# Kernel optimization log

Hardware: AMD Instinct MI355X
Metric: run time of the kernel (lower is better)

Reference implementation:

```python
import jax, jax.numpy as jnp
import numpy as np

B_, CIN, HH, WW = 2, 64, 64, 64
D_MODEL, D_INNER, D_STATE, DT_RANK, D_CONV = 64, 128, 16, 32, 3


def setup_inputs() -> dict:
    key = jax.random.key(0)
    ks = jax.random.split(key, 16)
    w = lambda k, shape: jax.random.normal(k, shape, jnp.float32) * 0.05
    # dt_proj bias init (torch: inv-softplus of dt sampled in [dt_min, dt_max])
    dt = jnp.exp(jax.random.uniform(ks[10], (D_INNER,)) * (np.log(0.1) - np.log(0.001)) + np.log(0.001))
    dt = jnp.clip(dt, 1e-4, None)
    inv_dt = dt + jnp.log(-jnp.expm1(-dt))
    A = jnp.tile(jnp.arange(1, D_STATE + 1, dtype=jnp.float32), (D_INNER, 1))
    return {
        "rgb_feat": jax.random.normal(ks[0], (B_, CIN, HH, WW), jnp.float32),
        "dte_feat": jax.random.normal(ks[1], (B_, CIN, HH, WW), jnp.float32),
        "conv1_w": w(ks[2], (D_MODEL, CIN)), "conv1_b": jnp.zeros((D_MODEL,), jnp.float32),
        "conv2_w": w(ks[3], (D_MODEL, CIN)), "conv2_b": jnp.zeros((D_MODEL,), jnp.float32),
        "conv3_w": w(ks[4], (CIN, D_MODEL)), "conv3_b": jnp.zeros((CIN,), jnp.float32),
        "norm_w": jnp.ones((D_MODEL,), jnp.float32),
        "in_proj_w": w(ks[5], (2 * D_INNER, D_MODEL)),
        "conv1d_w": w(ks[6], (D_INNER, D_CONV)), "conv1d_b": jnp.zeros((D_INNER,), jnp.float32),
        "x_proj_w": w(ks[7], (DT_RANK + 2 * D_STATE, D_INNER)),
        "dt_proj_w": jax.random.uniform(ks[8], (D_INNER, DT_RANK), jnp.float32, -DT_RANK ** -0.5, DT_RANK ** -0.5),
        "dt_proj_b": inv_dt,
        "A_log": jnp.log(A),
        "Dp": jnp.ones((D_INNER,), jnp.float32),
        "out_proj_w": w(ks[9], (D_MODEL, D_INNER)),
    }


def _conv1x1(x, w, b):
    return jnp.einsum('bchw,oc->bohw', x, w) + b[None, :, None, None]


def _rmsnorm(x, w, eps=1e-5):
    return x * jax.lax.rsqrt(jnp.mean(x * x, axis=-1, keepdims=True) + eps) * w


def _dwconv1d(x, w, b):
    # x: [B,L,D]; depthwise conv, kernel 3, padding 1 (same length)
    xt = jnp.transpose(x, (0, 2, 1))  # [B,D,L]
    y = jax.lax.conv_general_dilated(xt, w[:, None, :], (1,), [(1, 1)],
                                     dimension_numbers=('NCH', 'OIH', 'NCH'),
                                     feature_group_count=D_INNER)
    return jnp.transpose(y + b[None, :, None], (0, 2, 1))


def _mamba(x, h, p):
    # x: [B,L,d_model]
    xz = x @ p['in_proj_w'].T                      # [B,L,2*d_inner]
    xc, z = jnp.split(xz, 2, axis=-1)
    xc = jax.nn.silu(_dwconv1d(xc, p['conv1d_w'], p['conv1d_b']))
    A = -jnp.exp(p['A_log'])                       # [D,S]
    dbc = xc @ p['x_proj_w'].T                     # [B,L,dt_rank+2S]
    delta, Bm, Cm = jnp.split(dbc, [DT_RANK, DT_RANK + D_STATE], axis=-1)
    delta = jax.nn.softplus(delta @ p['dt_proj_w'].T + p['dt_proj_b'])  # [B,L,D]
    deltaA = jnp.exp(delta[..., None] * A)         # [B,L,D,S]
    BX = delta[..., None] * Bm[:, :, None, :] * xc[..., None]  # [B,L,D,S]
    h = deltaA * h + BX
    y = jnp.einsum('blds,bls->bld', h, Cm) + p['Dp'] * xc
    out = (y * jax.nn.silu(z)) @ p['out_proj_w'].T
    return out, h


def _residual_block(x4d, h, p):
    B, C, H, W = x4d.shape
    x = jnp.transpose(x4d.reshape(B, C, H * W), (0, 2, 1))  # [B,L,C]
    x = _rmsnorm(x, p['norm_w'])
    out, h = _mamba(x, h, p)
    out = out + x
    return jnp.transpose(out, (0, 2, 1)).reshape(B, C, H, W), h


def _rsfm(rgb_feat, dte_feat, conv1_w, conv1_b, conv2_w, conv2_b, conv3_w, conv3_b,
          norm_w, in_proj_w, conv1d_w, conv1d_b, x_proj_w, dt_proj_w, dt_proj_b,
          A_log, Dp, out_proj_w):
    p = dict(norm_w=norm_w, in_proj_w=in_proj_w, conv1d_w=conv1d_w, conv1d_b=conv1d_b,
             x_proj_w=x_proj_w, dt_proj_w=dt_proj_w, dt_proj_b=dt_proj_b,
             A_log=A_log, Dp=Dp, out_proj_w=out_proj_w)
    rgb = _conv1x1(rgb_feat, conv1_w, conv1_b)
    dte = _conv1x1(dte_feat, conv2_w, conv2_b)
    B = rgb.shape[0]
    h = jnp.zeros((B, HH * WW, D_INNER, D_STATE), jnp.float32)
    out1, h = _residual_block(rgb, h, p)
    out2, h = _residual_block(dte + out1, h, p)
    out3, h = _residual_block(rgb + out2, h, p)
    out4, h = _residual_block(dte + out3, h, p)
    out5, h = _residual_block(rgb + out4, h, p)
    out6, h = _residual_block(dte + out5, h, p)
    return _conv1x1(out6, conv3_w, conv3_b), h


def reference(rgb_feat, dte_feat, conv1_w, conv1_b, conv2_w, conv2_b, conv3_w, conv3_b,
              norm_w, in_proj_w, conv1d_w, conv1d_b, x_proj_w, dt_proj_w, dt_proj_b,
              A_log, Dp, out_proj_w):
    return _rsfm(rgb_feat, dte_feat, conv1_w, conv1_b, conv2_w, conv2_b, conv3_w, conv3_b,
                 norm_w, in_proj_w, conv1d_w, conv1d_b, x_proj_w, dt_proj_w, dt_proj_b,
                 A_log, Dp, out_proj_w)
```

## Files before the change

kernel.cpp:

```cpp
#include <hip/hip_runtime.h>

#define LSEQ 4096
#define NPOS 8192

__device__ __forceinline__ float silu_f(float x){ return x / (1.f + __expf(-x)); }
__device__ __forceinline__ float softplus_f(float x){
  return fmaxf(x, 0.f) + log1pf(__expf(-fabsf(x)));
}

__global__ __launch_bounds__(256) void k_prep(
    const float* __restrict__ ipw, const float* __restrict__ xpw,
    const float* __restrict__ dtw, const float* __restrict__ opw,
    const float* __restrict__ w1, const float* __restrict__ w2,
    const float* __restrict__ w3, const float* __restrict__ alog,
    float* __restrict__ ipT, float* __restrict__ xpT,
    float* __restrict__ dtT, float* __restrict__ opT,
    float* __restrict__ w1T, float* __restrict__ w2T,
    float* __restrict__ w3T, float* __restrict__ Aneg)
{
  int t = blockIdx.x * 256 + threadIdx.x;
  if (t < 16384){ int o = t >> 6, c = t & 63; ipT[c * 256 + o] = ipw[t]; }
  if (t < 8192){ int o = t >> 7, d = t & 127; xpT[d * 64 + o] = xpw[t]; }
  if (t < 4096){ int d = t >> 5, r = t & 31; dtT[r * 128 + d] = dtw[t]; }
  if (t < 8192){ int o = t >> 7, d = t & 127; opT[d * 64 + o] = opw[t]; }
  if (t < 4096){ int o = t >> 6, c = t & 63;
                 w1T[c*64+o] = w1[t]; w2T[c*64+o] = w2[t]; w3T[c*64+o] = w3[t]; }
  if (t < 2048){ Aneg[t] = -__expf(alog[t]); }
}

__global__ __launch_bounds__(256) void k_convin(
    const float* __restrict__ rgb, const float* __restrict__ dte,
    const float* __restrict__ w1T, const float* __restrict__ b1,
    const float* __restrict__ w2T, const float* __restrict__ b2,
    float* __restrict__ rgbp, float* __restrict__ dtep)
{
  int gw = (blockIdx.x * 256 + threadIdx.x) >> 6;
  int lane = threadIdx.x & 63;
  int which = gw >> 13;
  int n = gw & 8191;
  const float* x  = which ? dte : rgb;
  const float* wT = which ? w2T : w1T;
  const float* bb = which ? b2 : b1;
  float* o = which ? dtep : rgbp;
  int b = n >> 12, l = n & 4095;
  const float* xp = x + (size_t)b * 262144 + l;
  float acc = bb[lane];
  for (int c = 0; c < 64; c++)
    acc += wT[c*64 + lane] * xp[(size_t)c * 4096];
  o[(size_t)n*64 + lane] = acc;
}

__global__ __launch_bounds__(256) void k_pre(
    const float* __restrict__ xin, const float* __restrict__ normw,
    const float* __restrict__ ipT,
    float* __restrict__ xn, float* __restrict__ xcp, float* __restrict__ zs)
{
  __shared__ __align__(16) float xnl[4][8][64];
  const int wv = threadIdx.x >> 6, lane = threadIdx.x & 63;
  const int n0 = (blockIdx.x * 4 + wv) * 8;
  float nw = normw[lane];
  #pragma unroll 1
  for (int p = 0; p < 8; p++){
    int n = n0 + p;
    float v = xin[(size_t)n*64 + lane];
    float ss = v * v;
    for (int m = 32; m > 0; m >>= 1) ss += __shfl_xor(ss, m);
    v = v * rsqrtf(ss * (1.f/64.f) + 1e-5f) * nw;
    xn[(size_t)n*64 + lane] = v;
    xnl[wv][p][lane] = v;
  }
  float ac[8][4] = {};
  for (int c = 0; c < 64; c++){
    float w0 = ipT[c*256 + lane],       w1 = ipT[c*256 + 64 + lane];
    float w2 = ipT[c*256 + 128 + lane], w3 = ipT[c*256 + 192 + lane];
    #pragma unroll
    for (int p = 0; p < 8; p++){
      float xv = xnl[wv][p][c];
      ac[p][0] += w0*xv; ac[p][1] += w1*xv; ac[p][2] += w2*xv; ac[p][3] += w3*xv;
    }
  }
  #pragma unroll
  for (int p = 0; p < 8; p++){
    int n = n0 + p;
    xcp[(size_t)n*128 + lane]      = ac[p][0];
    xcp[(size_t)n*128 + 64 + lane] = ac[p][1];
    zs[(size_t)n*128 + lane]       = silu_f(ac[p][2]);
    zs[(size_t)n*128 + 64 + lane]  = silu_f(ac[p][3]);
  }
}

__global__ __launch_bounds__(256) void k_step(
    const float* __restrict__ xcpA, float* __restrict__ xcpB,
    float* __restrict__ zs, float* __restrict__ xn,
    float* __restrict__ h, const float* __restrict__ base_next,
    const float* __restrict__ xpT, const float* __restrict__ dtT,
    const float* __restrict__ opT, const float* __restrict__ Aneg,
    const float* __restrict__ c1w, const float* __restrict__ c1b,
    const float* __restrict__ dtb, const float* __restrict__ Dpw,
    const float* __restrict__ normw, const float* __restrict__ ipT,
    int hasH, int fusePre)
{
  __shared__ __align__(16) float xcl[4][4][128];
  __shared__ __align__(16) float dbl[4][4][64];
  __shared__ __align__(16) float yzl[4][4][128];
  __shared__ __align__(16) float xnl[4][4][64];
  const int wv = threadIdx.x >> 6, lane = threadIdx.x & 63;
  const int n0 = (blockIdx.x * 4 + wv) * 4;
  const int d0 = lane, d1 = 64 + lane;

  float cw00 = c1w[d0*3+0], cw01 = c1w[d0*3+1], cw02 = c1w[d0*3+2];
  float cw10 = c1w[d1*3+0], cw11 = c1w[d1*3+1], cw12 = c1w[d1*3+2];
  float cb0 = c1b[d0], cb1 = c1b[d1];

  float xc[4][2];
  #pragma unroll
  for (int p = 0; p < 4; p++){
    int n = n0 + p, l = n & (LSEQ-1);
    const float* xr = xcpA + (size_t)n * 128;
    float am0 = (l > 0) ? xr[d0 - 128] : 0.f;
    float am1 = (l > 0) ? xr[d1 - 128] : 0.f;
    float a00 = xr[d0], a01 = xr[d1];
    float ap0 = (l < LSEQ-1) ? xr[d0 + 128] : 0.f;
    float ap1 = (l < LSEQ-1) ? xr[d1 + 128] : 0.f;
    float v0 = silu_f(cw00*am0 + cw01*a00 + cw02*ap0 + cb0);
    float v1 = silu_f(cw10*am1 + cw11*a01 + cw12*ap1 + cb1);
    xc[p][0] = v0; xc[p][1] = v1;
    xcl[wv][p][d0] = v0; xcl[wv][p][d1] = v1;
  }

  float xa0=0.f, xa1=0.f, xa2=0.f, xa3=0.f;
  for (int d = 0; d < 128; d++){
    float w = xpT[d*64 + lane];
    xa0 += w * xcl[wv][0][d];
    xa1 += w * xcl[wv][1][d];
    xa2 += w * xcl[wv][2][d];
    xa3 += w * xcl[wv][3][d];
  }
  dbl[wv][0][lane]=xa0; dbl[wv][1][lane]=xa1; dbl[wv][2][lane]=xa2; dbl[wv][3][lane]=xa3;

  float tb0 = dtb[d0], tb1 = dtb[d1];
  float da[4][2];
  #pragma unroll
  for (int p = 0; p < 4; p++){ da[p][0]=tb0; da[p][1]=tb1; }
  for (int r = 0; r < 32; r++){
    float w0 = dtT[r*128 + d0];
    float w1 = dtT[r*128 + d1];
    #pragma unroll
    for (int p = 0; p < 4; p++){
      float bv = dbl[wv][p][r];
      da[p][0] += w0 * bv; da[p][1] += w1 * bv;
    }
  }
  float dl[4][2];
  #pragma unroll
  for (int p = 0; p < 4; p++){ dl[p][0]=softplus_f(da[p][0]); dl[p][1]=softplus_f(da[p][1]); }

  float an0[16], an1[16];
  {
    const float4* A0 = (const float4*)(Aneg + d0*16);
    const float4* A1 = (const float4*)(Aneg + d1*16);
    #pragma unroll
    for (int q = 0; q < 4; q++){
      float4 a = A0[q]; an0[q*4+0]=a.x; an0[q*4+1]=a.y; an0[q*4+2]=a.z; an0[q*4+3]=a.w;
      float4 b = A1[q]; an1[q*4+0]=b.x; an1[q*4+1]=b.y; an1[q*4+2]=b.z; an1[q*4+3]=b.w;
    }
  }
  float dp0 = Dpw[d0], dp1 = Dpw[d1];

  #pragma unroll 1
  for (int p = 0; p < 4; p++){
    int n = n0 + p;
    float Bm[16], Cm[16];
    {
      const float4* bb = (const float4*)&dbl[wv][p][32];
      const float4* cc = (const float4*)&dbl[wv][p][48];
      #pragma unroll
      for (int q = 0; q < 4; q++){
        float4 a = bb[q]; Bm[q*4+0]=a.x; Bm[q*4+1]=a.y; Bm[q*4+2]=a.z; Bm[q*4+3]=a.w;
        float4 b = cc[q]; Cm[q*4+0]=b.x; Cm[q*4+1]=b.y; Cm[q*4+2]=b.z; Cm[q*4+3]=b.w;
      }
    }
    float* hp0 = h + ((size_t)n*2048 + (size_t)d0*16);
    float* hp1 = h + ((size_t)n*2048 + (size_t)d1*16);
    float h0[16], h1[16];
    if (hasH){
      #pragma unroll
      for (int q = 0; q < 4; q++){
        float4 v = ((const float4*)hp0)[q];
        h0[q*4+0]=v.x; h0[q*4+1]=v.y; h0[q*4+2]=v.z; h0[q*4+3]=v.w;
        float4 w = ((const float4*)hp1)[q];
        h1[q*4+0]=w.x; h1[q*4+1]=w.y; h1[q*4+2]=w.z; h1[q*4+3]=w.w;
      }
    } else {
      #pragma unroll
      for (int s = 0; s < 16; s++){ h0[s]=0.f; h1[s]=0.f; }
    }
    float y0 = 0.f, y1 = 0.f;
    float dl0 = dl[p][0], dl1 = dl[p][1];
    float bx0 = dl0 * xc[p][0], bx1 = dl1 * xc[p][1];
    #pragma unroll
    for (int s = 0; s < 16; s++){
      h0[s] = __expf(dl0*an0[s])*h0[s] + bx0*Bm[s];
      y0 += h0[s]*Cm[s];
      h1[s] = __expf(dl1*an1[s])*h1[s] + bx1*Bm[s];
      y1 += h1[s]*Cm[s];
    }
    #pragma unroll
    for (int q = 0; q < 4; q++){
      float4 v; v.x=h0[q*4+0]; v.y=h0[q*4+1]; v.z=h0[q*4+2]; v.w=h0[q*4+3];
      ((float4*)hp0)[q] = v;
      float4 w; w.x=h1[q*4+0]; w.y=h1[q*4+1]; w.z=h1[q*4+2]; w.w=h1[q*4+3];
      ((float4*)hp1)[q] = w;
    }
    y0 += dp0 * xc[p][0];
    y1 += dp1 * xc[p][1];
    yzl[wv][p][d0] = y0 * zs[(size_t)n*128 + d0];
    yzl[wv][p][d1] = y1 * zs[(size_t)n*128 + d1];
  }

  float oa[4] = {0.f,0.f,0.f,0.f};
  for (int d = 0; d < 128; d++){
    float w = opT[d*64 + lane];
    oa[0] += w * yzl[wv][0][d];
    oa[1] += w * yzl[wv][1][d];
    oa[2] += w * yzl[wv][2][d];
    oa[3] += w * yzl[wv][3][d];
  }

  float nw = normw[lane];
  if (fusePre){
    #pragma unroll 1
    for (int p = 0; p < 4; p++){
      int n = n0 + p;
      float v = oa[p] + xn[(size_t)n*64 + lane] + base_next[(size_t)n*64 + lane];
      float ss = v * v;
      for (int m = 32; m > 0; m >>= 1) ss += __shfl_xor(ss, m);
      v = v * rsqrtf(ss * (1.f/64.f) + 1e-5f) * nw;
      xn[(size_t)n*64 + lane] = v;
      xnl[wv][p][lane] = v;
    }
    float ac[4][4] = {};
    for (int c = 0; c < 64; c++){
      float w0 = ipT[c*256 + lane],       w1 = ipT[c*256 + 64 + lane];
      float w2 = ipT[c*256 + 128 + lane], w3 = ipT[c*256 + 192 + lane];
      #pragma unroll
      for (int p = 0; p < 4; p++){
        float xv = xnl[wv][p][c];
        ac[p][0] += w0*xv; ac[p][1] += w1*xv; ac[p][2] += w2*xv; ac[p][3] += w3*xv;
      }
    }
    #pragma unroll
    for (int p = 0; p < 4; p++){
      int n = n0 + p;
      xcpB[(size_t)n*128 + lane]      = ac[p][0];
      xcpB[(size_t)n*128 + 64 + lane] = ac[p][1];
      zs[(size_t)n*128 + lane]        = silu_f(ac[p][2]);
      zs[(size_t)n*128 + 64 + lane]   = silu_f(ac[p][3]);
    }
  } else {
    #pragma unroll
    for (int p = 0; p < 4; p++){
      int n = n0 + p;
      xcpB[(size_t)n*64 + lane] = oa[p] + xn[(size_t)n*64 + lane];
    }
  }
}

__global__ __launch_bounds__(256) void k_conv3(
    const float* __restrict__ out6, const float* __restrict__ w3T,
    const float* __restrict__ b3, float* __restrict__ out)
{
  __shared__ __align__(16) float t[64][65];
  const int tid = threadIdx.x;
  const int n0 = blockIdx.x * 64;
  #pragma unroll
  for (int i = 0; i < 16; i++){
    int idx = tid + 256*i;
    int r = idx >> 6, c = idx & 63;
    t[r][c] = out6[(size_t)(n0 + r)*64 + c];
  }
  __syncthreads();
  const int i = tid & 63;
  const int cb = (tid >> 6) * 16;
  float acc[16];
  #pragma unroll
  for (int j = 0; j < 16; j++) acc[j] = b3[cb + j];
  for (int o = 0; o < 64; o++){
    float xv = t[i][o];
    #pragma unroll
    for (int j = 0; j < 16; j++) acc[j] += w3T[o*64 + cb + j] * xv;
  }
  const int b = n0 >> 12;
  const int l = (n0 & 4095) + i;
  #pragma unroll
  for (int j = 0; j < 16; j++)
    out[(size_t)b*262144 + (size_t)(cb + j)*4096 + l] = acc[j];
}

extern "C" void kernel_launch(void* const* d_in, const int* in_sizes, int n_in,
                              void* d_out, int out_size, void* d_ws, size_t ws_size,
                              hipStream_t stream)
{
  const float* rgb  = (const float*)d_in[0];
  const float* dte  = (const float*)d_in[1];
  const float* w1   = (const float*)d_in[2];
  const float* b1   = (const float*)d_in[3];
  const float* w2   = (const float*)d_in[4];
  const float* b2   = (const float*)d_in[5];
  const float* w3   = (const float*)d_in[6];
  const float* b3   = (const float*)d_in[7];
  const float* nrm  = (const float*)d_in[8];
  const float* ipw  = (const float*)d_in[9];
  const float* c1w  = (const float*)d_in[10];
  const float* c1b  = (const float*)d_in[11];
  const float* xpw  = (const float*)d_in[12];
  const float* dtw  = (const float*)d_in[13];
  const float* dtb  = (const float*)d_in[14];
  const float* alog = (const float*)d_in[15];
  const float* Dpw  = (const float*)d_in[16];
  const float* opw  = (const float*)d_in[17];

  float* out  = (float*)d_out;
  float* hbuf = out + 524288;

  float* ws   = (float*)d_ws;
  float* rgbp = ws;
  float* dtep = ws + 524288;
  float* xnb  = ws + 1048576;
  float* zsb  = ws + 1572864;
  float* xcp0 = ws + 2621440;
  float* xcp1 = ws + 3670016;
  float* Aneg = ws + 4718592;
  float* wb   = ws + 4720640;
  float* ipT = wb;
  float* xpT = wb + 16384;
  float* dtT = wb + 24576;
  float* opT = wb + 28672;
  float* w1T = wb + 36864;
  float* w2T = wb + 40960;
  float* w3T = wb + 45056;

  k_prep<<<64, 256, 0, stream>>>(ipw, xpw, dtw, opw, w1, w2, w3, alog,
                                 ipT, xpT, dtT, opT, w1T, w2T, w3T, Aneg);
  k_convin<<<4096, 256, 0, stream>>>(rgb, dte, w1T, b1, w2T, b2, rgbp, dtep);
  k_pre<<<256, 256, 0, stream>>>(rgbp, nrm, ipT, xnb, xcp0, zsb);

  float* xa[2] = {xcp0, xcp1};
  for (int k = 0; k < 6; k++){
    const float* base = (k == 5) ? nullptr : ((k & 1) ? rgbp : dtep);
    k_step<<<512, 256, 0, stream>>>(xa[k & 1], xa[(k & 1) ^ 1], zsb, xnb, hbuf, base,
                                    xpT, dtT, opT, Aneg, c1w, c1b, dtb, Dpw, nrm, ipT,
                                    (k > 0) ? 1 : 0, (k < 5) ? 1 : 0);
  }
  k_conv3<<<128, 256, 0, stream>>>(xcp0, w3T, b3, out);
}
```

Baseline: 417.4 us.

## Store intermediate SSM state in bf16, tile input conv, and halve positions per wave

The 64 MB-scale hidden state h is kept in a bf16 workspace between residual blocks, and only the final block writes fp32 to the output. This roughly halves the dominant HBM traffic of the step kernels. The input 1x1 convs are rewritten to stage a 64-position tile in LDS and write coalesced outputs. k_pre and k_step now process 2 positions per wave instead of 8/4, launching more blocks for better occupancy. Rounding h to bf16 between blocks adds precision error that may break tolerance.

Measured after the change: 364.4 us. 12.7% less time.

```diff
diff --git a/kernel.cpp b/kernel.cpp
--- a/kernel.cpp
+++ b/kernel.cpp
@@ -1,8 +1,27 @@
 #include <hip/hip_runtime.h>
+
+typedef unsigned short u16;
+typedef unsigned int u32;
 
 #define LSEQ 4096
 #define NPOS 8192
 
+__device__ __forceinline__ float bf2f(u16 u){
+  union { u32 i; float f; } v; v.i = ((u32)u) << 16; return v.f;
+}
+__device__ __forceinline__ u16 f2bf(float f){
+  union { float f; u32 i; } v; v.f = f;
+  u32 x = v.i;
+  return (u16)((x + 0x7fffu + ((x >> 16) & 1u)) >> 16);
+}
+__device__ __forceinline__ float2 up2(u32 u){
+  union { u32 i; float f; } a, b;
+  a.i = u << 16; b.i = u & 0xffff0000u;
+  float2 r; r.x = a.f; r.y = b.f; return r;
+}
+__device__ __forceinline__ u32 pk2(float a, float b){
+  return (u32)f2bf(a) | ((u32)f2bf(b) << 16);
+}
 __device__ __forceinline__ float silu_f(float x){ return x / (1.f + __expf(-x)); }
 __device__ __forceinline__ float softplus_f(float x){
   return fmaxf(x, 0.f) + log1pf(__expf(-fabsf(x)));
@@ -34,20 +53,44 @@
     const float* __restrict__ w2T, const float* __restrict__ b2,
     float* __restrict__ rgbp, float* __restrict__ dtep)
 {
-  int gw = (blockIdx.x * 256 + threadIdx.x) >> 6;
-  int lane = threadIdx.x & 63;
-  int which = gw >> 13;
-  int n = gw & 8191;
-  const float* x  = which ? dte : rgb;
-  const float* wT = which ? w2T : w1T;
-  const float* bb = which ? b2 : b1;
+  __shared__ __align__(16) float xt[64][64];
+  __shared__ __align__(16) float ot[64][65];
+  const int tid = threadIdx.x;
+  const int which = blockIdx.x & 1;
+  const int n0 = (blockIdx.x >> 1) * 64;
+  const int b = n0 >> 12, l0 = n0 & 4095;
+  const float* src = which ? dte : rgb;
+  const float* wT  = which ? w2T : w1T;
+  const float* bb  = which ? b2 : b1;
   float* o = which ? dtep : rgbp;
-  int b = n >> 12, l = n & 4095;
-  const float* xp = x + (size_t)b * 262144 + l;
-  float acc = bb[lane];
-  for (int c = 0; c < 64; c++)
-    acc += wT[c*64 + lane] * xp[(size_t)c * 4096];
-  o[(size_t)n*64 + lane] = acc;
+
+  #pragma unroll
+  for (int j = 0; j < 16; j++){
+    int idx = tid + 256 * j;
+    int c = idx >> 6, p = idx & 63;
+    xt[c][p] = src[(size_t)b * 262144 + (size_t)c * 4096 + l0 + p];
+  }
+  __syncthreads();
+
+  const int pos = tid & 63;
+  const int cb  = (tid >> 6) * 16;
+  float acc[16];
+  #pragma unroll
+  for (int j = 0; j < 16; j++) acc[j] = bb[cb + j];
+  for (int c = 0; c < 64; c++){
+    float xv = xt[c][pos];
+    #pragma unroll
+    for (int j = 0; j < 16; j++) acc[j] += wT[c*64 + cb + j] * xv;
+  }
+  #pragma unroll
+  for (int j = 0; j < 16; j++) ot[pos][cb + j] = acc[j];
+  __syncthreads();
+  #pragma unroll
+  for (int j = 0; j < 16; j++){
+    int idx = tid + 256 * j;
+    int p = idx >> 6, c = idx & 63;
+    o[(size_t)(n0 + p)*64 + c] = ot[p][c];
+  }
 }
 
 __global__ __launch_bounds__(256) void k_pre(
@@ -55,12 +98,12 @@
     const float* __restrict__ ipT,
     float* __restrict__ xn, float* __restrict__ xcp, float* __restrict__ zs)
 {
-  __shared__ __align__(16) float xnl[4][8][64];
+  __shared__ __align__(16) float xnl[4][2][64];
   const int wv = threadIdx.x >> 6, lane = threadIdx.x & 63;
-  const int n0 = (blockIdx.x * 4 + wv) * 8;
+  const int n0 = (blockIdx.x * 4 + wv) * 2;
   float nw = normw[lane];
-  #pragma unroll 1
-  for (int p = 0; p < 8; p++){
+  #pragma unroll
+  for (int p = 0; p < 2; p++){
     int n = n0 + p;
     float v = xin[(size_t)n*64 + lane];
     float ss = v * v;
@@ -69,18 +112,18 @@
     xn[(size_t)n*64 + lane] = v;
     xnl[wv][p][lane] = v;
   }
-  float ac[8][4] = {};
+  float ac[2][4] = {};
   for (int c = 0; c < 64; c++){
     float w0 = ipT[c*256 + lane],       w1 = ipT[c*256 + 64 + lane];
     float w2 = ipT[c*256 + 128 + lane], w3 = ipT[c*256 + 192 + lane];
     #pragma unroll
-    for (int p = 0; p < 8; p++){
+    for (int p = 0; p < 2; p++){
       float xv = xnl[wv][p][c];
       ac[p][0] += w0*xv; ac[p][1] += w1*xv; ac[p][2] += w2*xv; ac[p][3] += w3*xv;
     }
   }
   #pragma unroll
-  for (int p = 0; p < 8; p++){
+  for (int p = 0; p < 2; p++){
     int n = n0 + p;
     xcp[(size_t)n*128 + lane]      = ac[p][0];
     xcp[(size_t)n*128 + 64 + lane] = ac[p][1];
@@ -92,7 +135,8 @@
 __global__ __launch_bounds__(256) void k_step(
     const float* __restrict__ xcpA, float* __restrict__ xcpB,
     float* __restrict__ zs, float* __restrict__ xn,
-    float* __restrict__ h, const float* __restrict__ base_next,
+    u16* __restrict__ hbf, float* __restrict__ hfin,
+    const float* __restrict__ base_next,
     const float* __restrict__ xpT, const float* __restrict__ dtT,
     const float* __restrict__ opT, const float* __restrict__ Aneg,
     const float* __restrict__ c1w, const float* __restrict__ c1b,
@@ -100,60 +144,59 @@
     const float* __restrict__ normw, const float* __restrict__ ipT,
     int hasH, int fusePre)
 {
-  __shared__ __align__(16) float xcl[4][4][128];
-  __shared__ __align__(16) float dbl[4][4][64];
-  __shared__ __align__(16) float yzl[4][4][128];
-  __shared__ __align__(16) float xnl[4][4][64];
+  __shared__ __align__(16) float xcl[4][2][128];
+  __shared__ __align__(16) float dbl[4][2][64];
+  __shared__ __align__(16) float yzl[4][2][128];
+  __shared__ __align__(16) float xnl[4][2][64];
   const int wv = threadIdx.x >> 6, lane = threadIdx.x & 63;
-  const int n0 = (blockIdx.x * 4 + wv) * 4;
+  const int n0 = (blockIdx.x * 4 + wv) * 2;
   const int d0 = lane, d1 = 64 + lane;
 
   float cw00 = c1w[d0*3+0], cw01 = c1w[d0*3+1], cw02 = c1w[d0*3+2];
   float cw10 = c1w[d1*3+0], cw11 = c1w[d1*3+1], cw12 = c1w[d1*3+2];
   float cb0 = c1b[d0], cb1 = c1b[d1];
 
-  float xc[4][2];
-  #pragma unroll
-  for (int p = 0; p < 4; p++){
-    int n = n0 + p, l = n & (LSEQ-1);
+  float xc0[2], xc1[2];
+  #pragma unroll
+  for (int p = 0; p < 2; p++){
+    int n = n0 + p, l = n & 4095;
     const float* xr = xcpA + (size_t)n * 128;
-    float am0 = (l > 0) ? xr[d0 - 128] : 0.f;
-    float am1 = (l > 0) ? xr[d1 - 128] : 0.f;
+    float am0 = 0.f, am1 = 0.f, ap0 = 0.f, ap1 = 0.f;
+    if (l > 0)    { am0 = xr[d0 - 128]; am1 = xr[d1 - 128]; }
     float a00 = xr[d0], a01 = xr[d1];
-    float ap0 = (l < LSEQ-1) ? xr[d0 + 128] : 0.f;
-    float ap1 = (l < LSEQ-1) ? xr[d1 + 128] : 0.f;
+    if (l < 4095) { ap0 = xr[d0 + 128]; ap1 = xr[d1 + 128]; }
     float v0 = silu_f(cw00*am0 + cw01*a00 + cw02*ap0 + cb0);
     float v1 = silu_f(cw10*am1 + cw11*a01 + cw12*ap1 + cb1);
-    xc[p][0] = v0; xc[p][1] = v1;
+    xc0[p] = v0; xc1[p] = v1;
     xcl[wv][p][d0] = v0; xcl[wv][p][d1] = v1;
   }
 
-  float xa0=0.f, xa1=0.f, xa2=0.f, xa3=0.f;
-  for (int d = 0; d < 128; d++){
-    float w = xpT[d*64 + lane];
-    xa0 += w * xcl[wv][0][d];
-    xa1 += w * xcl[wv][1][d];
-    xa2 += w * xcl[wv][2][d];
-    xa3 += w * xcl[wv][3][d];
-  }
-  dbl[wv][0][lane]=xa0; dbl[wv][1][lane]=xa1; dbl[wv][2][lane]=xa2; dbl[wv][3][lane]=xa3;
-
-  float tb0 = dtb[d0], tb1 = dtb[d1];
-  float da[4][2];
-  #pragma unroll
-  for (int p = 0; p < 4; p++){ da[p][0]=tb0; da[p][1]=tb1; }
-  for (int r = 0; r < 32; r++){
-    float w0 = dtT[r*128 + d0];
-    float w1 = dtT[r*128 + d1];
-    #pragma unroll
-    for (int p = 0; p < 4; p++){
-      float bv = dbl[wv][p][r];
-      da[p][0] += w0 * bv; da[p][1] += w1 * bv;
-    }
-  }
-  float dl[4][2];
-  #pragma unroll
-  for (int p = 0; p < 4; p++){ dl[p][0]=softplus_f(da[p][0]); dl[p][1]=softplus_f(da[p][1]); }
+  {
+    float xa[2] = {0,0};
+    for (int d = 0; d < 128; d++){
+      float w = xpT[d*64 + lane];
+      #pragma unroll
+      for (int p = 0; p < 2; p++) xa[p] += w * xcl[wv][p][d];
+    }
+    #pragma unroll
+    for (int p = 0; p < 2; p++) dbl[wv][p][lane] = xa[p];
+  }
+
+  float dl0[2], dl1[2];
+  {
+    float tb0 = dtb[d0], tb1 = dtb[d1];
+    float da0[2] = {tb0, tb0}, da1[2] = {tb1, tb1};
+    for (int r = 0; r < 32; r++){
+      float w0 = dtT[r*128 + d0], w1 = dtT[r*128 + d1];
+      #pragma unroll
+      for (int p = 0; p < 2; p++){
+        float bv = dbl[wv][p][r];
+        da0[p] += w0 * bv; da1[p] += w1 * bv;
+      }
+    }
+    #pragma unroll
+    for (int p = 0; p < 2; p++){ dl0[p] = softplus_f(da0[p]); dl1[p] = softplus_f(da1[p]); }
+  }
 
   float an0[16], an1[16];
   {
@@ -168,7 +211,7 @@
   float dp0 = Dpw[d0], dp1 = Dpw[d1];
 
   #pragma unroll 1
-  for (int p = 0; p < 4; p++){
+  for (int p = 0; p < 2; p++){
     int n = n0 + p;
     float Bm[16], Cm[16];
     {
@@ -180,57 +223,74 @@
         float4 b = cc[q]; Cm[q*4+0]=b.x; Cm[q*4+1]=b.y; Cm[q*4+2]=b.z; Cm[q*4+3]=b.w;
       }
     }
-    float* hp0 = h + ((size_t)n*2048 + (size_t)d0*16);
-    float* hp1 = h + ((size_t)n*2048 + (size_t)d1*16);
+    u16* hp0 = hbf + ((size_t)n*2048 + (size_t)d0*16);
+    u16* hp1 = hbf + ((size_t)n*2048 + (size_t)d1*16);
     float h0[16], h1[16];
     if (hasH){
       #pragma unroll
+      for (int q = 0; q < 2; q++){
+        uint4 v = ((const uint4*)hp0)[q];
+        float2 t0=up2(v.x), t1=up2(v.y), t2=up2(v.z), t3=up2(v.w);
+        h0[q*8+0]=t0.x; h0[q*8+1]=t0.y; h0[q*8+2]=t1.x; h0[q*8+3]=t1.y;
+        h0[q*8+4]=t2.x; h0[q*8+5]=t2.y; h0[q*8+6]=t3.x; h0[q*8+7]=t3.y;
+        uint4 w = ((const uint4*)hp1)[q];
+        float2 s0=up2(w.x), s1=up2(w.y), s2=up2(w.z), s3=up2(w.w);
+        h1[q*8+0]=s0.x; h1[q*8+1]=s0.y; h1[q*8+2]=s1.x; h1[q*8+3]=s1.y;
+        h1[q*8+4]=s2.x; h1[q*8+5]=s2.y; h1[q*8+6]=s3.x; h1[q*8+7]=s3.y;
+      }
+    } else {
+      #pragma unroll
+      for (int s = 0; s < 16; s++){ h0[s]=0.f; h1[s]=0.f; }
+    }
+    float y0 = 0.f, y1 = 0.f;
+    float bx0 = dl0[p] * xc0[p], bx1 = dl1[p] * xc1[p];
+    #pragma unroll
+    for (int s = 0; s < 16; s++){
+      h0[s] = __expf(dl0[p]*an0[s])*h0[s] + bx0*Bm[s];
+      y0 = fmaf(h0[s], Cm[s], y0);
+      h1[s] = __expf(dl1[p]*an1[s])*h1[s] + bx1*Bm[s];
+      y1 = fmaf(h1[s], Cm[s], y1);
+    }
+    if (fusePre){
+      #pragma unroll
+      for (int q = 0; q < 2; q++){
+        uint4 v;
+        v.x = pk2(h0[q*8+0], h0[q*8+1]); v.y = pk2(h0[q*8+2], h0[q*8+3]);
+        v.z = pk2(h0[q*8+4], h0[q*8+5]); v.w = pk2(h0[q*8+6], h0[q*8+7]);
+        ((uint4*)hp0)[q] = v;
+        uint4 w;
+        w.x = pk2(h1[q*8+0], h1[q*8+1]); w.y = pk2(h1[q*8+2], h1[q*8+3]);
+        w.z = pk2(h1[q*8+4], h1[q*8+5]); w.w = pk2(h1[q*8+6], h1[q*8+7]);
+        ((uint4*)hp1)[q] = w;
+      }
+    } else {
+      float4* f0 = (float4*)(hfin + (size_t)n*2048 + (size_t)d0*16);
+      float4* f1 = (float4*)(hfin + (size_t)n*2048 + (size_t)d1*16);
+      #pragma unroll
       for (int q = 0; q < 4; q++){
-        float4 v = ((const float4*)hp0)[q];
-        h0[q*4+0]=v.x; h0[q*4+1]=v.y; h0[q*4+2]=v.z; h0[q*4+3]=v.w;
-        float4 w = ((const float4*)hp1)[q];
-        h1[q*4+0]=w.x; h1[q*4+1]=w.y; h1[q*4+2]=w.z; h1[q*4+3]=w.w;
-      }
-    } else {
-      #pragma unroll
-      for (int s = 0; s < 16; s++){ h0[s]=0.f; h1[s]=0.f; }
-    }
-    float y0 = 0.f, y1 = 0.f;
-    float dl0 = dl[p][0], dl1 = dl[p][1];
-    float bx0 = dl0 * xc[p][0], bx1 = dl1 * xc[p][1];
-    #pragma unroll
-    for (int s = 0; s < 16; s++){
-      h0[s] = __expf(dl0*an0[s])*h0[s] + bx0*Bm[s];
-      y0 += h0[s]*Cm[s];
-      h1[s] = __expf(dl1*an1[s])*h1[s] + bx1*Bm[s];
-      y1 += h1[s]*Cm[s];
-    }
-    #pragma unroll
-    for (int q = 0; q < 4; q++){
-      float4 v; v.x=h0[q*4+0]; v.y=h0[q*4+1]; v.z=h0[q*4+2]; v.w=h0[q*4+3];
-      ((float4*)hp0)[q] = v;
-      float4 w; w.x=h1[q*4+0]; w.y=h1[q*4+1]; w.z=h1[q*4+2]; w.w=h1[q*4+3];
-      ((float4*)hp1)[q] = w;
-    }
-    y0 += dp0 * xc[p][0];
-    y1 += dp1 * xc[p][1];
+        float4 v; v.x=h0[q*4+0]; v.y=h0[q*4+1]; v.z=h0[q*4+2]; v.w=h0[q*4+3];
+        f0[q] = v;
+        float4 w; w.x=h1[q*4+0]; w.y=h1[q*4+1]; w.z=h1[q*4+2]; w.w=h1[q*4+3];
+        f1[q] = w;
+      }
+    }
+    y0 += dp0 * xc0[p];
+    y1 += dp1 * xc1[p];
     yzl[wv][p][d0] = y0 * zs[(size_t)n*128 + d0];
     yzl[wv][p][d1] = y1 * zs[(size_t)n*128 + d1];
   }
 
-  float oa[4] = {0.f,0.f,0.f,0.f};
+  float oa[2] = {0,0};
   for (int d = 0; d < 128; d++){
     float w = opT[d*64 + lane];
-    oa[0] += w * yzl[wv][0][d];
-    oa[1] += w * yzl[wv][1][d];
-    oa[2] += w * yzl[wv][2][d];
-    oa[3] += w * yzl[wv][3][d];
+    #pragma unroll
+    for (int p = 0; p < 2; p++) oa[p] += w * yzl[wv][p][d];
   }
 
   float nw = normw[lane];
   if (fusePre){
-    #pragma unroll 1
-    for (int p = 0; p < 4; p++){
+    #pragma unroll
+    for (int p = 0; p < 2; p++){
       int n = n0 + p;
       float v = oa[p] + xn[(size_t)n*64 + lane] + base_next[(size_t)n*64 + lane];
       float ss = v * v;
@@ -239,18 +299,18 @@
       xn[(size_t)n*64 + lane] = v;
       xnl[wv][p][lane] = v;
     }
-    float ac[4][4] = {};
+    float ac[2][4] = {};
     for (int c = 0; c < 64; c++){
       float w0 = ipT[c*256 + lane],       w1 = ipT[c*256 + 64 + lane];
       float w2 = ipT[c*256 + 128 + lane], w3 = ipT[c*256 + 192 + lane];
       #pragma unroll
-      for (int p = 0; p < 4; p++){
+      for (int p = 0; p < 2; p++){
         float xv = xnl[wv][p][c];
         ac[p][0] += w0*xv; ac[p][1] += w1*xv; ac[p][2] += w2*xv; ac[p][3] += w3*xv;
       }
     }
     #pragma unroll
-    for (int p = 0; p < 4; p++){
+    for (int p = 0; p < 2; p++){
       int n = n0 + p;
       xcpB[(size_t)n*128 + lane]      = ac[p][0];
       xcpB[(size_t)n*128 + 64 + lane] = ac[p][1];
@@ -259,7 +319,7 @@
     }
   } else {
     #pragma unroll
-    for (int p = 0; p < 4; p++){
+    for (int p = 0; p < 2; p++){
       int n = n0 + p;
       xcpB[(size_t)n*64 + lane] = oa[p] + xn[(size_t)n*64 + lane];
     }
@@ -320,37 +380,39 @@
   const float* Dpw  = (const float*)d_in[16];
   const float* opw  = (const float*)d_in[17];
 
-  float* out  = (float*)d_out;
-  float* hbuf = out + 524288;
+  float* outc = (float*)d_out;
+  float* hfin = outc + 524288;
 
   float* ws   = (float*)d_ws;
-  float* rgbp = ws;
-  float* dtep = ws + 524288;
-  float* xnb  = ws + 1048576;
-  float* zsb  = ws + 1572864;
-  float* xcp0 = ws + 2621440;
-  float* xcp1 = ws + 3670016;
-  float* Aneg = ws + 4718592;
-  float* wb   = ws + 4720640;
-  float* ipT = wb;
-  float* xpT = wb + 16384;
-  float* dtT = wb + 24576;
-  float* opT = wb + 28672;
-  float* w1T = wb + 36864;
-  float* w2T = wb + 40960;
-  float* w3T = wb + 45056;
+  float* xcp0 = ws;
+  float* xcp1 = ws + 1048576;
+  float* rgbp = ws + 2097152;
+  float* dtep = ws + 2621440;
+  float* xnb  = ws + 3145728;
+  float* zsb  = ws + 3670016;
+  float* wb   = ws + 4718592;
+  float* ipT  = wb;
+  float* xpT  = wb + 16384;
+  float* dtT  = wb + 24576;
+  float* opT  = wb + 28672;
+  float* w1T  = wb + 36864;
+  float* w2T  = wb + 40960;
+  float* w3T  = wb + 45056;
+  float* Aneg = wb + 49152;
+  u16*   hbf  = (u16*)(ws + 4769792);
 
   k_prep<<<64, 256, 0, stream>>>(ipw, xpw, dtw, opw, w1, w2, w3, alog,
                                  ipT, xpT, dtT, opT, w1T, w2T, w3T, Aneg);
-  k_convin<<<4096, 256, 0, stream>>>(rgb, dte, w1T, b1, w2T, b2, rgbp, dtep);
-  k_pre<<<256, 256, 0, stream>>>(rgbp, nrm, ipT, xnb, xcp0, zsb);
+  k_convin<<<256, 256, 0, stream>>>(rgb, dte, w1T, b1, w2T, b2, rgbp, dtep);
+  k_pre<<<1024, 256, 0, stream>>>(rgbp, nrm, ipT, xnb, xcp0, zsb);
 
   float* xa[2] = {xcp0, xcp1};
   for (int k = 0; k < 6; k++){
-    const float* base = (k == 5) ? nullptr : ((k & 1) ? rgbp : dtep);
-    k_step<<<512, 256, 0, stream>>>(xa[k & 1], xa[(k & 1) ^ 1], zsb, xnb, hbuf, base,
-                                    xpT, dtT, opT, Aneg, c1w, c1b, dtb, Dpw, nrm, ipT,
-                                    (k > 0) ? 1 : 0, (k < 5) ? 1 : 0);
-  }
-  k_conv3<<<128, 256, 0, stream>>>(xcp0, w3T, b3, out);
-}
+    const float* base = (k == 5) ? rgbp  : ((k & 1) ? rgbp : dtep);
+    k_step<<<1024, 256, 0, stream>>>(xa[k & 1], xa[(k & 1) ^ 1], zsb, xnb,
+                                     hbf, hfin, base,
+                                     xpT, dtT, opT, Aneg, c1w, c1b, dtb, Dpw,
+                                     nrm, ipT, (k > 0) ? 1 : 0, (k < 5) ? 1 : 0);
+  }
+  k_conv3<<<128, 256, 0, stream>>>(xcp0, w3T, b3, outc);
+}
```
